# Performance work log

Measured on AMD Instinct MI355X. Metric: run time of the kernel, lower is better.

## Reference

```python
import jax, jax.numpy as jnp
import numpy as np

N_NODES = 50000
N_EDGES = 800000
IN_CH = 128
HID = 32
HEADS = 8
OUT_CH = 40
NEG_SLOPE = 0.2


def setup_inputs() -> dict:
    key = jax.random.key(0)
    ks = jax.random.split(key, 12)
    g = lambda k, shape, fan: (jax.random.normal(k, shape, jnp.float32) / np.sqrt(fan).astype(np.float32))
    return {
        "x": jax.random.normal(ks[0], (N_NODES, IN_CH), jnp.float32),
        "edge_index": jax.random.randint(ks[1], (2, N_EDGES), 0, N_NODES, jnp.int64),
        "W1l": g(ks[2], (IN_CH, HEADS * HID), IN_CH),
        "W1r": g(ks[3], (IN_CH, HEADS * HID), IN_CH),
        "att1": g(ks[4], (HEADS, HID), HID),
        "b1": jnp.zeros((HEADS * HID,), jnp.float32),
        "W2l": g(ks[5], (HEADS * HID, HID), HEADS * HID),
        "W2r": g(ks[6], (HEADS * HID, HID), HEADS * HID),
        "att2": g(ks[7], (1, HID), HID),
        "b2": jnp.zeros((HID,), jnp.float32),
        "Wc": g(ks[8], (HID + IN_CH, OUT_CH), HID + IN_CH),
        "bc": jnp.zeros((OUT_CH,), jnp.float32),
    }


def _gatv2(x, ei, Wl, Wr, att, b, heads, ch):
    # GATv2Conv (concat=True): e_ij = att . LeakyReLU(Wl x_j + Wr x_i)
    n = x.shape[0]
    src, dst = ei[0], ei[1]  # message flows src(j) -> dst(i)
    xl = (x @ Wl).reshape(n, heads, ch)  # source transform
    xr = (x @ Wr).reshape(n, heads, ch)  # target transform
    e = jax.nn.leaky_relu(xl[src] + xr[dst], NEG_SLOPE)  # [E, H, C]
    score = jnp.einsum("ehc,hc->eh", e, att)             # [E, H]
    # per-target-node segment softmax (stable)
    m = jax.ops.segment_max(score, dst, num_segments=n)
    alpha = jnp.exp(score - m[dst])
    denom = jax.ops.segment_sum(alpha, dst, num_segments=n)
    alpha = alpha / denom[dst]
    out = jax.ops.segment_sum(alpha[:, :, None] * xl[src], dst, num_segments=n)
    return out.reshape(n, heads * ch) + b


def reference(x, edge_index, W1l, W1r, att1, b1, W2l, W2r, att2, b2, Wc, bc):
    n = x.shape[0]
    ar = jnp.arange(n, dtype=edge_index.dtype)
    ei = jnp.concatenate([edge_index, jnp.stack([ar, ar])], axis=1)  # add self-loops
    h1 = jax.nn.elu(_gatv2(x, ei, W1l, W1r, att1, b1, HEADS, HID))
    h2 = jax.nn.elu(_gatv2(h1, ei, W2l, W2r, att2, b2, 1, HID))
    combined = jnp.concatenate([h2, x], axis=1)
    return combined @ Wc + bc
```

## Files before the change

### kernel.cpp

```cpp
#include <hip/hip_runtime.h>
#include <cstdint>
#include <cstddef>
#include <math.h>

#define NN 50000
#define INCH 128
#define HIDC 32
#define NHEAD 8
#define OUTC 40
#define SLOT 64

typedef unsigned short ushort_t;
using bf16x8 = __attribute__((ext_vector_type(8))) short;
using f32x4  = __attribute__((ext_vector_type(4))) float;
using f32x2  = __attribute__((ext_vector_type(2))) float;

__device__ __forceinline__ float bf2f(unsigned short h) {
    return __uint_as_float(((unsigned int)h) << 16);
}
__device__ __forceinline__ unsigned short f2bf(float f) {
    unsigned int u = __float_as_uint(f);
    u = u + 0x7FFFu + ((u >> 16) & 1u);
    return (unsigned short)(u >> 16);
}
__device__ __forceinline__ float lo16(unsigned int u) { return __uint_as_float(u << 16); }
__device__ __forceinline__ float hi16(unsigned int u) { return __uint_as_float(u & 0xffff0000u); }
__device__ __forceinline__ f32x2 up2(unsigned int u) {
    f32x2 r; r.x = lo16(u); r.y = hi16(u); return r;
}
__device__ __forceinline__ f32x2 pabs(f32x2 v) {
    return __builtin_elementwise_max(v, -v);
}

__global__ __launch_bounds__(256) void prep_all(
    const float* __restrict__ x, ushort_t* __restrict__ xb, int total8,
    const float* __restrict__ W1l, const float* __restrict__ W1r,
    const float* __restrict__ W2l, const float* __restrict__ W2r,
    const float* __restrict__ Wc,
    ushort_t* __restrict__ BT1, ushort_t* __restrict__ BT2, ushort_t* __restrict__ BTc,
    int* __restrict__ deg, int n, int CX) {
    const int blk = blockIdx.x;
    const int tid = threadIdx.x;
    if (blk < CX) {
        int i = blk * 256 + tid;
        if (i >= total8) return;
        float4 f0 = *(const float4*)(x + (size_t)i * 8);
        float4 f1 = *(const float4*)(x + (size_t)i * 8 + 4);
        ushort4 u0, u1;
        u0.x = f2bf(f0.x); u0.y = f2bf(f0.y); u0.z = f2bf(f0.z); u0.w = f2bf(f0.w);
        u1.x = f2bf(f1.x); u1.y = f2bf(f1.y); u1.z = f2bf(f1.z); u1.w = f2bf(f1.w);
        *(ushort4*)(xb + (size_t)i * 8) = u0;
        *(ushort4*)(xb + (size_t)i * 8 + 4) = u1;
    } else if (blk < CX + 616) {
        int b = blk - CX, k = tid;
        if (b < 512) {
            if (k < 128) {
                float v = (b < 256) ? W1l[(size_t)k * 256 + b] : W1r[(size_t)k * 256 + (b - 256)];
                BT1[(size_t)b * 128 + k] = f2bf(v);
            }
        } else if (b < 576) {
            int c = b - 512;
            float v = (c < 32) ? W2l[(size_t)k * 32 + c] : W2r[(size_t)k * 32 + (c - 32)];
            BT2[(size_t)c * 256 + k] = f2bf(v);
        } else {
            int c = b - 576;
            if (k < 160) BTc[(size_t)c * 160 + k] = f2bf(Wc[(size_t)k * 40 + c]);
        }
    } else {
        int i = (blk - CX - 616) * 256 + tid;
        if (i < n) deg[i] = 0;
    }
}

__global__ __launch_bounds__(256) void g1_scatter(
    const ushort_t* __restrict__ xb, const ushort_t* __restrict__ BT1,
    const float* __restrict__ att,
    ushort_t* __restrict__ xl1, ushort_t* __restrict__ xr1,
    float* __restrict__ dl, float* __restrict__ dr, int M,
    const int* __restrict__ ei, int E, int n,
    int* __restrict__ deg, int* __restrict__ csr_src, int G1) {
    const int blk = blockIdx.x;
    const int tid = threadIdx.x;
    if (blk >= G1) {
        int e = (blk - G1) * 256 + tid;
        if (e >= E + n) return;
        int src, dst;
        if (e < E) { src = ei[e]; dst = ei[E + e]; } else { src = dst = e - E; }
        int pos = atomicAdd(&deg[dst], 1);
        if (pos < SLOT) csr_src[((size_t)dst << 6) + pos] = src;
        return;
    }
    __shared__ ushort_t As[128][72];
    __shared__ ushort_t Bs[128][72];
    const int rowBase = (blk >> 2) * 128;
    const int bx = blk & 3;
    const int c0 = bx * 128;
    const int wid = tid >> 6, lane = tid & 63;
    const int wr = wid >> 1, wc = wid & 1;
    const int l15 = lane & 15, l4 = lane >> 4;
    f32x4 acc[4][4];
    #pragma unroll
    for (int i = 0; i < 4; ++i)
        #pragma unroll
        for (int j = 0; j < 4; ++j)
            #pragma unroll
            for (int q = 0; q < 4; ++q) acc[i][j][q] = 0.f;

    for (int c = 0; c < 2; ++c) {
        #pragma unroll
        for (int h = 0; h < 4; ++h) {
            int idx = h * 256 + tid;
            int r = idx >> 3, seg = idx & 7;
            int row = rowBase + r;
            uint4 v = {0, 0, 0, 0};
            if (row < M) v = *(const uint4*)(xb + (size_t)row * 128 + c * 64 + seg * 8);
            *(uint4*)&As[r][seg * 8] = v;
            *(uint4*)&Bs[r][seg * 8] = *(const uint4*)(BT1 + (size_t)(c0 + r) * 128 + c * 64 + seg * 8);
        }
        __syncthreads();
        #pragma unroll
        for (int kk = 0; kk < 2; ++kk) {
            bf16x8 a[4], b[4];
            #pragma unroll
            for (int f = 0; f < 4; ++f) {
                a[f] = *(const bf16x8*)&As[wr * 64 + f * 16 + l15][kk * 32 + l4 * 8];
                b[f] = *(const bf16x8*)&Bs[wc * 64 + f * 16 + l15][kk * 32 + l4 * 8];
            }
            #pragma unroll
            for (int i = 0; i < 4; ++i)
                #pragma unroll
                for (int j = 0; j < 4; ++j)
                    acc[i][j] = __builtin_amdgcn_mfma_f32_16x16x32_bf16(a[i], b[j], acc[i][j], 0, 0, 0);
        }
        __syncthreads();
    }
    ushort_t* __restrict__ cout = (bx < 2) ? xl1 : xr1;
    const int colBase = (bx & 1) * 128;
    #pragma unroll
    for (int i = 0; i < 4; ++i)
        #pragma unroll
        for (int r = 0; r < 4; ++r) {
            int row = rowBase + wr * 64 + i * 16 + l4 * 4 + r;
            if (row >= M) continue;
            #pragma unroll
            for (int j = 0; j < 4; ++j) {
                int col = colBase + wc * 64 + j * 16 + l15;
                cout[(size_t)row * 256 + col] = f2bf(acc[i][j][r]);
            }
        }
    float attv[4];
    #pragma unroll
    for (int j = 0; j < 4; ++j)
        attv[j] = att[(bx & 1) * 128 + wc * 64 + j * 16 + l15];
    float* __restrict__ dst = (bx < 2) ? dl : dr;
    const int headA = (bx & 1) * 4 + wc * 2;
    #pragma unroll
    for (int i = 0; i < 4; ++i)
        #pragma unroll
        for (int r = 0; r < 4; ++r) {
            float s0 = fmaf(acc[i][1][r], attv[1], acc[i][0][r] * attv[0]);
            float s1 = fmaf(acc[i][3][r], attv[3], acc[i][2][r] * attv[2]);
            s0 += __shfl_xor(s0, 1); s1 += __shfl_xor(s1, 1);
            s0 += __shfl_xor(s0, 2); s1 += __shfl_xor(s1, 2);
            s0 += __shfl_xor(s0, 4); s1 += __shfl_xor(s1, 4);
            s0 += __shfl_xor(s0, 8); s1 += __shfl_xor(s1, 8);
            if (l15 == 0) {
                int row = rowBase + wr * 64 + i * 16 + l4 * 4 + r;
                if (row < M) {
                    dst[(size_t)row * 8 + headA] = s0;
                    dst[(size_t)row * 8 + headA + 1] = s1;
                }
            }
        }
}

__global__ __launch_bounds__(256) void gat_agg1(
    const ushort_t* __restrict__ xl, const ushort_t* __restrict__ xr,
    const float* __restrict__ dl, const float* __restrict__ dr,
    const float* __restrict__ att, const float* __restrict__ b,
    const int* __restrict__ degArr, const int* __restrict__ csr_src,
    ushort_t* __restrict__ h1) {
    const int lane = threadIdx.x & 63;
    const int i = blockIdx.x * 4 + (threadIdx.x >> 6);
    const int half = lane >> 5;
    const int sl = lane & 31;
    const int head = sl >> 2;

    uint4 xv = *(const uint4*)(xr + (size_t)i * 256 + sl * 8);
    const f32x2 xr01 = up2(xv.x), xr23 = up2(xv.y), xr45 = up2(xv.z), xr67 = up2(xv.w);
    const float4 atA = *(const float4*)(att + sl * 8);
    const float4 atB = *(const float4*)(att + sl * 8 + 4);
    f32x2 at01, at23, at45, at67;
    at01.x = atA.x; at01.y = atA.y; at23.x = atA.z; at23.y = atA.w;
    at45.x = atB.x; at45.y = atB.y; at67.x = atB.z; at67.y = atB.w;
    const float cbase = 0.6f * dr[(size_t)i * 8 + head];
    int degv = degArr[i]; degv = degv < SLOT ? degv : SLOT;
    const int p0 = i << 6;
    const int p1 = p0 + degv;
    const int pfull = p0 + (degv & ~3);

    float dsum = 0.f;
    f32x2 a01 = {0.f, 0.f}, a23 = {0.f, 0.f}, a45 = {0.f, 0.f}, a67 = {0.f, 0.f};

    int pcA = p0 + half;     pcA = pcA < p1 ? pcA : p1 - 1;
    int jA = csr_src[pcA];
    uint4 uvA = *(const uint4*)(xl + (size_t)jA * 256 + sl * 8);
    float dlA = dl[(size_t)jA * 8 + head];
    int pcB = p0 + 2 + half; pcB = pcB < p1 ? pcB : p1 - 1;
    int jB = csr_src[pcB];
    uint4 uvB = *(const uint4*)(xl + (size_t)jB * 256 + sl * 8);
    float dlB = dl[(size_t)jB * 8 + head];

    for (int p = p0; p < pfull; p += 4) {
        {
            f32x2 v01 = up2(uvA.x), v23 = up2(uvA.y), v45 = up2(uvA.z), v67 = up2(uvA.w);
            float base = fmaf(0.6f, dlA, cbase);
            int nxt = p + 4 + half; int pc = nxt < p1 ? nxt : p1 - 1;
            int jn = csr_src[pc];
            uvA = *(const uint4*)(xl + (size_t)jn * 256 + sl * 8);
            dlA = dl[(size_t)jn * 8 + head];
            f32x2 q2 = at01 * pabs(v01 + xr01);
            q2 = __builtin_elementwise_fma(at23, pabs(v23 + xr23), q2);
            q2 = __builtin_elementwise_fma(at45, pabs(v45 + xr45), q2);
            q2 = __builtin_elementwise_fma(at67, pabs(v67 + xr67), q2);
            float q = q2.x + q2.y;
            q += __shfl_xor(q, 1);
            q += __shfl_xor(q, 2);
            float w = __expf(fmaf(0.4f, q, base));
            dsum += w;
            f32x2 w2; w2.x = w; w2.y = w;
            a01 = __builtin_elementwise_fma(w2, v01, a01);
            a23 = __builtin_elementwise_fma(w2, v23, a23);
            a45 = __builtin_elementwise_fma(w2, v45, a45);
            a67 = __builtin_elementwise_fma(w2, v67, a67);
        }
        {
            f32x2 v01 = up2(uvB.x), v23 = up2(uvB.y), v45 = up2(uvB.z), v67 = up2(uvB.w);
            float base = fmaf(0.6f, dlB, cbase);
            int nxt = p + 6 + half; int pc = nxt < p1 ? nxt : p1 - 1;
            int jn = csr_src[pc];
            uvB = *(const uint4*)(xl + (size_t)jn * 256 + sl * 8);
            dlB = dl[(size_t)jn * 8 + head];
            f32x2 q2 = at01 * pabs(v01 + xr01);
            q2 = __builtin_elementwise_fma(at23, pabs(v23 + xr23), q2);
            q2 = __builtin_elementwise_fma(at45, pabs(v45 + xr45), q2);
            q2 = __builtin_elementwise_fma(at67, pabs(v67 + xr67), q2);
            float q = q2.x + q2.y;
            q += __shfl_xor(q, 1);
            q += __shfl_xor(q, 2);
            float w = __expf(fmaf(0.4f, q, base));
            dsum += w;
            f32x2 w2; w2.x = w; w2.y = w;
            a01 = __builtin_elementwise_fma(w2, v01, a01);
            a23 = __builtin_elementwise_fma(w2, v23, a23);
            a45 = __builtin_elementwise_fma(w2, v45, a45);
            a67 = __builtin_elementwise_fma(w2, v67, a67);
        }
    }
    const int t = degv & 3;
    if (t) {
        {
            const bool val = half < t;
            f32x2 v01 = up2(uvA.x), v23 = up2(uvA.y), v45 = up2(uvA.z), v67 = up2(uvA.w);
            float base = fmaf(0.6f, dlA, cbase);
            f32x2 q2 = at01 * pabs(v01 + xr01);
            q2 = __builtin_elementwise_fma(at23, pabs(v23 + xr23), q2);
            q2 = __builtin_elementwise_fma(at45, pabs(v45 + xr45), q2);
            q2 = __builtin_elementwise_fma(at67, pabs(v67 + xr67), q2);
            float q = q2.x + q2.y;
            q += __shfl_xor(q, 1);
            q += __shfl_xor(q, 2);
            float w = val ? __expf(fmaf(0.4f, q, base)) : 0.f;
            dsum += w;
            f32x2 w2; w2.x = w; w2.y = w;
            a01 = __builtin_elementwise_fma(w2, v01, a01);
            a23 = __builtin_elementwise_fma(w2, v23, a23);
            a45 = __builtin_elementwise_fma(w2, v45, a45);
            a67 = __builtin_elementwise_fma(w2, v67, a67);
        }
        if (t > 2) {
            const bool val = (2 + half) < t;
            f32x2 v01 = up2(uvB.x), v23 = up2(uvB.y), v45 = up2(uvB.z), v67 = up2(uvB.w);
            float base = fmaf(0.6f, dlB, cbase);
            f32x2 q2 = at01 * pabs(v01 + xr01);
            q2 = __builtin_elementwise_fma(at23, pabs(v23 + xr23), q2);
            q2 = __builtin_elementwise_fma(at45, pabs(v45 + xr45), q2);
            q2 = __builtin_elementwise_fma(at67, pabs(v67 + xr67), q2);
            float q = q2.x + q2.y;
            q += __shfl_xor(q, 1);
            q += __shfl_xor(q, 2);
            float w = val ? __expf(fmaf(0.4f, q, base)) : 0.f;
            dsum += w;
            f32x2 w2; w2.x = w; w2.y = w;
            a01 = __builtin_elementwise_fma(w2, v01, a01);
            a23 = __builtin_elementwise_fma(w2, v23, a23);
            a45 = __builtin_elementwise_fma(w2, v45, a45);
            a67 = __builtin_elementwise_fma(w2, v67, a67);
        }
    }
    dsum += __shfl_xor(dsum, 32);
    a01.x += __shfl_xor(a01.x, 32); a01.y += __shfl_xor(a01.y, 32);
    a23.x += __shfl_xor(a23.x, 32); a23.y += __shfl_xor(a23.y, 32);
    a45.x += __shfl_xor(a45.x, 32); a45.y += __shfl_xor(a45.y, 32);
    a67.x += __shfl_xor(a67.x, 32); a67.y += __shfl_xor(a67.y, 32);

    if (half == 0) {
        const float4 bA = *(const float4*)(b + sl * 8);
        const float4 bB = *(const float4*)(b + sl * 8 + 4);
        float inv = 1.f / dsum;
        float o0 = fmaf(a01.x, inv, bA.x), o1 = fmaf(a01.y, inv, bA.y);
        float o2 = fmaf(a23.x, inv, bA.z), o3 = fmaf(a23.y, inv, bA.w);
        float o4 = fmaf(a45.x, inv, bB.x), o5 = fmaf(a45.y, inv, bB.y);
        float o6 = fmaf(a67.x, inv, bB.z), o7 = fmaf(a67.y, inv, bB.w);
        o0 = o0 > 0.f ? o0 : __expf(o0) - 1.f;
        o1 = o1 > 0.f ? o1 : __expf(o1) - 1.f;
        o2 = o2 > 0.f ? o2 : __expf(o2) - 1.f;
        o3 = o3 > 0.f ? o3 : __expf(o3) - 1.f;
        o4 = o4 > 0.f ? o4 : __expf(o4) - 1.f;
        o5 = o5 > 0.f ? o5 : __expf(o5) - 1.f;
        o6 = o6 > 0.f ? o6 : __expf(o6) - 1.f;
        o7 = o7 > 0.f ? o7 : __expf(o7) - 1.f;
        uint4 ov;
        ov.x = ((unsigned)f2bf(o1) << 16) | f2bf(o0);
        ov.y = ((unsigned)f2bf(o3) << 16) | f2bf(o2);
        ov.z = ((unsigned)f2bf(o5) << 16) | f2bf(o4);
        ov.w = ((unsigned)f2bf(o7) << 16) | f2bf(o6);
        *(uint4*)(h1 + (size_t)i * 256 + sl * 8) = ov;
    }
}

__global__ __launch_bounds__(256) void gemm2_mfma(
    const ushort_t* __restrict__ h1, const ushort_t* __restrict__ BT2,
    const float* __restrict__ att,
    ushort_t* __restrict__ xl2, ushort_t* __restrict__ xr2,
    float* __restrict__ dl2, float* __restrict__ dr2, int M) {
    __shared__ ushort_t As[128][72];
    __shared__ ushort_t Bs[64][264];
    const int tid = threadIdx.x;
    const int rowBase = blockIdx.x * 128;
    const int wid = tid >> 6, lane = tid & 63;
    const int l15 = lane & 15, l4 = lane >> 4;
    #pragma unroll
    for (int h = 0; h < 8; ++h) {
        int idx = h * 256 + tid;
        int r = idx >> 5, seg = idx & 31;
        *(uint4*)&Bs[r][seg * 8] = *(const uint4*)(BT2 + (size_t)r * 256 + seg * 8);
    }
    f32x4 acc[2][4];
    #pragma unroll
    for (int i = 0; i < 2; ++i)
        #pragma unroll
        for (int j = 0; j < 4; ++j)
            #pragma unroll
            for (int q = 0; q < 4; ++q) acc[i][j][q] = 0.f;

    for (int c = 0; c < 4; ++c) {
        #pragma unroll
        for (int h = 0; h < 4; ++h) {
            int idx = h * 256 + tid;
            int r = idx >> 3, seg = idx & 7;
            int row = rowBase + r;
            uint4 v = {0, 0, 0, 0};
            if (row < M) v = *(const uint4*)(h1 + (size_t)row * 256 + c * 64 + seg * 8);
            *(uint4*)&As[r][seg * 8] = v;
        }
        __syncthreads();
        #pragma unroll
        for (int kk = 0; kk < 2; ++kk) {
            bf16x8 a[2], b[4];
            #pragma unroll
            for (int f = 0; f < 2; ++f)
                a[f] = *(const bf16x8*)&As[wid * 32 + f * 16 + l15][kk * 32 + l4 * 8];
            #pragma unroll
            for (int f = 0; f < 4; ++f)
                b[f] = *(const bf16x8*)&Bs[f * 16 + l15][c * 64 + kk * 32 + l4 * 8];
            #pragma unroll
            for (int i = 0; i < 2; ++i)
                #pragma unroll
                for (int j = 0; j < 4; ++j)
                    acc[i][j] = __builtin_amdgcn_mfma_f32_16x16x32_bf16(a[i], b[j], acc[i][j], 0, 0, 0);
        }
        __syncthreads();
    }
    #pragma unroll
    for (int i = 0; i < 2; ++i)
        #pragma unroll
        for (int r = 0; r < 4; ++r) {
            int row = rowBase + wid * 32 + i * 16 + l4 * 4 + r;
            if (row >= M) continue;
            #pragma unroll
            for (int j = 0; j < 4; ++j) {
                int col = j * 16 + l15;
                if (col < 32) xl2[(size_t)row * 32 + col] = f2bf(acc[i][j][r]);
                else          xr2[(size_t)row * 32 + (col - 32)] = f2bf(acc[i][j][r]);
            }
        }
    float attv[4];
    #pragma unroll
    for (int j = 0; j < 4; ++j)
        attv[j] = att[(j * 16 + l15) & 31];
    #pragma unroll
    for (int i = 0; i < 2; ++i)
        #pragma unroll
        for (int r = 0; r < 4; ++r) {
            float s0 = fmaf(acc[i][1][r], attv[1], acc[i][0][r] * attv[0]);
            float s1 = fmaf(acc[i][3][r], attv[3], acc[i][2][r] * attv[2]);
            s0 += __shfl_xor(s0, 1); s1 += __shfl_xor(s1, 1);
            s0 += __shfl_xor(s0, 2); s1 += __shfl_xor(s1, 2);
            s0 += __shfl_xor(s0, 4); s1 += __shfl_xor(s1, 4);
            s0 += __shfl_xor(s0, 8); s1 += __shfl_xor(s1, 8);
            if (l15 == 0) {
                int row = rowBase + wid * 32 + i * 16 + l4 * 4 + r;
                if (row < M) {
                    dl2[row] = s0;
                    dr2[row] = s1;
                }
            }
        }
}

__global__ __launch_bounds__(256) void gat_agg2(
    const ushort_t* __restrict__ xl, const ushort_t* __restrict__ xr,
    const float* __restrict__ dl, const float* __restrict__ dr,
    const float* __restrict__ att, const float* __restrict__ b,
    const int* __restrict__ degArr, const int* __restrict__ csr_src,
    ushort_t* __restrict__ h2) {
    const int lane = threadIdx.x & 63;
    const int i = blockIdx.x * 4 + (threadIdx.x >> 6);
    const int g = lane >> 3;
    const int h8 = lane & 7;
    uint2 xv = *(const uint2*)(xr + (size_t)i * 32 + h8 * 4);
    const f32x2 xr01 = up2(xv.x), xr23 = up2(xv.y);
    const float4 at = *(const float4*)(att + h8 * 4);
    f32x2 at01, at23;
    at01.x = at.x; at01.y = at.y; at23.x = at.z; at23.y = at.w;
    const float cbase = 0.6f * dr[i];
    int degv = degArr[i]; degv = degv < SLOT ? degv : SLOT;
    const int p0 = i << 6;
    const int p1 = p0 + degv;
    const int pfull = p0 + (degv & ~15);
    float dsum = 0.f;
    f32x2 a01 = {0.f, 0.f}, a23 = {0.f, 0.f};

    int pcA = p0 + g;     pcA = pcA < p1 ? pcA : p1 - 1;
    int jA = csr_src[pcA];
    uint2 uvA = *(const uint2*)(xl + (size_t)jA * 32 + h8 * 4);
    float dlA = dl[jA];
    int pcB = p0 + g + 8; pcB = pcB < p1 ? pcB : p1 - 1;
    int jB = csr_src[pcB];
    uint2 uvB = *(const uint2*)(xl + (size_t)jB * 32 + h8 * 4);
    float dlB = dl[jB];

    for (int p = p0; p < pfull; p += 16) {
        {
            f32x2 v01 = up2(uvA.x), v23 = up2(uvA.y);
            float base = fmaf(0.6f, dlA, cbase);
            int nxt = p + g + 16; int pc = nxt < p1 ? nxt : p1 - 1;
            int jn = csr_src[pc];
            uvA = *(const uint2*)(xl + (size_t)jn * 32 + h8 * 4);
            dlA = dl[jn];
            f32x2 q2 = at01 * pabs(v01 + xr01);
            q2 = __builtin_elementwise_fma(at23, pabs(v23 + xr23), q2);
            float q = q2.x + q2.y;
            q += __shfl_xor(q, 1);
            q += __shfl_xor(q, 2);
            q += __shfl_xor(q, 4);
            float w = __expf(fmaf(0.4f, q, base));
            dsum += w;
            f32x2 w2; w2.x = w; w2.y = w;
            a01 = __builtin_elementwise_fma(w2, v01, a01);
            a23 = __builtin_elementwise_fma(w2, v23, a23);
        }
        {
            f32x2 v01 = up2(uvB.x), v23 = up2(uvB.y);
            float base = fmaf(0.6f, dlB, cbase);
            int nxt = p + g + 24; int pc = nxt < p1 ? nxt : p1 - 1;
            int jn = csr_src[pc];
            uvB = *(const uint2*)(xl + (size_t)jn * 32 + h8 * 4);
            dlB = dl[jn];
            f32x2 q2 = at01 * pabs(v01 + xr01);
            q2 = __builtin_elementwise_fma(at23, pabs(v23 + xr23), q2);
            float q = q2.x + q2.y;
            q += __shfl_xor(q, 1);
            q += __shfl_xor(q, 2);
            q += __shfl_xor(q, 4);
            float w = __expf(fmaf(0.4f, q, base));
            dsum += w;
            f32x2 w2; w2.x = w; w2.y = w;
            a01 = __builtin_elementwise_fma(w2, v01, a01);
            a23 = __builtin_elementwise_fma(w2, v23, a23);
        }
    }
    const int t = degv & 15;
    if (t) {
        {
            const bool val = g < t;
            f32x2 v01 = up2(uvA.x), v23 = up2(uvA.y);
            float base = fmaf(0.6f, dlA, cbase);
            f32x2 q2 = at01 * pabs(v01 + xr01);
            q2 = __builtin_elementwise_fma(at23, pabs(v23 + xr23), q2);
            float q = q2.x + q2.y;
            q += __shfl_xor(q, 1);
            q += __shfl_xor(q, 2);
            q += __shfl_xor(q, 4);
            float w = val ? __expf(fmaf(0.4f, q, base)) : 0.f;
            dsum += w;
            f32x2 w2; w2.x = w; w2.y = w;
            a01 = __builtin_elementwise_fma(w2, v01, a01);
            a23 = __builtin_elementwise_fma(w2, v23, a23);
        }
        if (t > 8) {
            const bool val = (g + 8) < t;
            f32x2 v01 = up2(uvB.x), v23 = up2(uvB.y);
            float base = fmaf(0.6f, dlB, cbase);
            f32x2 q2 = at01 * pabs(v01 + xr01);
            q2 = __builtin_elementwise_fma(at23, pabs(v23 + xr23), q2);
            float q = q2.x + q2.y;
            q += __shfl_xor(q, 1);
            q += __shfl_xor(q, 2);
            q += __shfl_xor(q, 4);
            float w = val ? __expf(fmaf(0.4f, q, base)) : 0.f;
            dsum += w;
            f32x2 w2; w2.x = w; w2.y = w;
            a01 = __builtin_elementwise_fma(w2, v01, a01);
            a23 = __builtin_elementwise_fma(w2, v23, a23);
        }
    }
    dsum += __shfl_xor(dsum, 8);  dsum += __shfl_xor(dsum, 16);  dsum += __shfl_xor(dsum, 32);
    a01.x += __shfl_xor(a01.x, 8); a01.x += __shfl_xor(a01.x, 16); a01.x += __shfl_xor(a01.x, 32);
    a01.y += __shfl_xor(a01.y, 8); a01.y += __shfl_xor(a01.y, 16); a01.y += __shfl_xor(a01.y, 32);
    a23.x += __shfl_xor(a23.x, 8); a23.x += __shfl_xor(a23.x, 16); a23.x += __shfl_xor(a23.x, 32);
    a23.y += __shfl_xor(a23.y, 8); a23.y += __shfl_xor(a23.y, 16); a23.y += __shfl_xor(a23.y, 32);
    if (g == 0) {
        const float4 bb = *(const float4*)(b + h8 * 4);
        float inv = 1.f / dsum;
        float o0 = fmaf(a01.x, inv, bb.x);
        float o1 = fmaf(a01.y, inv, bb.y);
        float o2 = fmaf(a23.x, inv, bb.z);
        float o3 = fmaf(a23.y, inv, bb.w);
        o0 = o0 > 0.f ? o0 : __expf(o0) - 1.f;
        o1 = o1 > 0.f ? o1 : __expf(o1) - 1.f;
        o2 = o2 > 0.f ? o2 : __expf(o2) - 1.f;
        o3 = o3 > 0.f ? o3 : __expf(o3) - 1.f;
        uint2 ov;
        ov.x = ((unsigned)f2bf(o1) << 16) | f2bf(o0);
        ov.y = ((unsigned)f2bf(o3) << 16) | f2bf(o2);
        *(uint2*)(h2 + (size_t)i * 32 + h8 * 4) = ov;
    }
}

__global__ __launch_bounds__(256) void final_mfma(
    const ushort_t* __restrict__ h2, const ushort_t* __restrict__ xb,
    const ushort_t* __restrict__ BTc, const float* __restrict__ bc,
    float* __restrict__ out, int M) {
    __shared__ ushort_t As[128][168];
    __shared__ ushort_t Bs[48][168];
    const int tid = threadIdx.x;
    const int rowBase = blockIdx.x * 128;
    const int wid = tid >> 6, lane = tid & 63;
    const int l15 = lane & 15, l4 = lane >> 4;
    #pragma unroll
    for (int h = 0; h < 4; ++h) {
        int idx = h * 256 + tid;
        if (idx < 960) {
            int r = idx / 20, seg = idx % 20;
            uint4 v = {0, 0, 0, 0};
            if (r < 40) v = *(const uint4*)(BTc + (size_t)r * 160 + seg * 8);
            *(uint4*)&Bs[r][seg * 8] = v;
        }
    }
    #pragma unroll
    for (int h = 0; h < 10; ++h) {
        int idx = h * 256 + tid;
        int r = idx / 20, seg = idx % 20;
        int row = rowBase + r;
        uint4 v = {0, 0, 0, 0};
        if (row < M)
            v = (seg < 4) ? *(const uint4*)(h2 + (size_t)row * 32 + seg * 8)
                          : *(const uint4*)(xb + (size_t)row * 128 + (seg - 4) * 8);
        *(uint4*)&As[r][seg * 8] = v;
    }
    __syncthreads();
    f32x4 acc[2][3];
    #pragma unroll
    for (int i = 0; i < 2; ++i)
        #pragma unroll
        for (int j = 0; j < 3; ++j)
            #pragma unroll
            for (int q = 0; q < 4; ++q) acc[i][j][q] = 0.f;
    #pragma unroll
    for (int kk = 0; kk < 5; ++kk) {
        bf16x8 a[2], b[3];
        #pragma unroll
        for (int f = 0; f < 2; ++f)
            a[f] = *(const bf16x8*)&As[wid * 32 + f * 16 + l15][kk * 32 + l4 * 8];
        #pragma unroll
        for (int f = 0; f < 3; ++f)
            b[f] = *(const bf16x8*)&Bs[f * 16 + l15][kk * 32 + l4 * 8];
        #pragma unroll
        for (int i = 0; i < 2; ++i)
            #pragma unroll
            for (int j = 0; j < 3; ++j)
                acc[i][j] = __builtin_amdgcn_mfma_f32_16x16x32_bf16(a[i], b[j], acc[i][j], 0, 0, 0);
    }
    #pragma unroll
    for (int i = 0; i < 2; ++i)
        #pragma unroll
        for (int r = 0; r < 4; ++r) {
            int row = rowBase + wid * 32 + i * 16 + l4 * 4 + r;
            if (row >= M) continue;
            #pragma unroll
            for (int j = 0; j < 3; ++j) {
                int col = j * 16 + l15;
                if (col < 40) out[(size_t)row * 40 + col] = acc[i][j][r] + bc[col];
            }
        }
}


extern "C" void kernel_launch(void* const* d_in, const int* in_sizes, int n_in,
                              void* d_out, int out_size, void* d_ws, size_t ws_size,
                              hipStream_t stream) {
    const float* x    = (const float*)d_in[0];
    const int*   ei   = (const int*)d_in[1];
    const float* W1l  = (const float*)d_in[2];
    const float* W1r  = (const float*)d_in[3];
    const float* att1 = (const float*)d_in[4];
    const float* b1   = (const float*)d_in[5];
    const float* W2l  = (const float*)d_in[6];
    const float* W2r  = (const float*)d_in[7];
    const float* att2 = (const float*)d_in[8];
    const float* b2   = (const float*)d_in[9];
    const float* Wc   = (const float*)d_in[10];
    const float* bc   = (const float*)d_in[11];
    float* out = (float*)d_out;

    const int n  = NN;
    const int E  = in_sizes[1] / 2;
    const int TE = E + n;
    const int CX = (n * 128 / 8 + 255) / 256;
    const int DZ = (n + 255) / 256;
    const int CD = (TE + 255) / 256;
    const int G1 = 4 * ((n + 127) / 128);

    char* ws = (char*)d_ws;
    size_t off = 0;
    auto alloc = [&](size_t bytes) { void* p = ws + off; off += (bytes + 255) & ~(size_t)255; return p; };
    ushort_t* xb   = (ushort_t*)alloc((size_t)n * 128 * 2);
    ushort_t* xl1  = (ushort_t*)alloc((size_t)n * 256 * 2);
    ushort_t* xr1  = (ushort_t*)alloc((size_t)n * 256 * 2);
    ushort_t* h1   = (ushort_t*)alloc((size_t)n * 256 * 2);
    ushort_t* xl2  = (ushort_t*)alloc((size_t)n * 32 * 2);
    ushort_t* xr2  = (ushort_t*)alloc((size_t)n * 32 * 2);
    ushort_t* h2   = (ushort_t*)alloc((size_t)n * 32 * 2);
    ushort_t* BT1  = (ushort_t*)alloc(512 * 128 * 2);
    ushort_t* BT2  = (ushort_t*)alloc(64 * 256 * 2);
    ushort_t* BTc  = (ushort_t*)alloc(40 * 160 * 2);
    float* dl1 = (float*)alloc((size_t)n * 8 * 4);
    float* dr1 = (float*)alloc((size_t)n * 8 * 4);
    float* dl2 = (float*)alloc((size_t)n * 4);
    float* dr2 = (float*)alloc((size_t)n * 4);
    int* deg     = (int*)alloc((size_t)n * 4);
    int* csr_src = (int*)alloc((size_t)n * SLOT * 4);

    prep_all<<<CX + 616 + DZ, 256, 0, stream>>>(x, xb, n * 128 / 8,
        W1l, W1r, W2l, W2r, Wc, BT1, BT2, BTc, deg, n, CX);

    g1_scatter<<<G1 + CD, 256, 0, stream>>>(xb, BT1, att1, xl1, xr1, dl1, dr1, n,
                                            ei, E, n, deg, csr_src, G1);

    gat_agg1<<<n / 4, 256, 0, stream>>>(xl1, xr1, dl1, dr1, att1, b1, deg, csr_src, h1);

    gemm2_mfma<<<(n + 127) / 128, 256, 0, stream>>>(h1, BT2, att2, xl2, xr2, dl2, dr2, n);

    gat_agg2<<<n / 4, 256, 0, stream>>>(xl2, xr2, dl2, dr2, att2, b2, deg, csr_src, h2);

    final_mfma<<<(n + 127) / 128, 256, 0, stream>>>(h2, xb, BTc, bc, out, n);
}
```

Measured before the change: 312.5 us.

## Split edge scatter from GEMM1 kernel and batch atomics per thread

Separates the fused GEMM1 plus edge-scatter kernel into two launches: a scatter kernel where each thread handles four edges with their loads and atomics issued together, and a standalone GEMM kernel on a 2D grid. Self-loops are now written in prep (deg initialised to 1 with slot 0 set), so the scatter skips n atomics. This removes divergent block roles in one kernel but adds an extra launch and serialises scatter before GEMM on the stream.

```diff
diff --git a/kernel.cpp b/kernel.cpp
--- a/kernel.cpp
+++ b/kernel.cpp
@@ -38,7 +38,7 @@
     const float* __restrict__ W2l, const float* __restrict__ W2r,
     const float* __restrict__ Wc,
     ushort_t* __restrict__ BT1, ushort_t* __restrict__ BT2, ushort_t* __restrict__ BTc,
-    int* __restrict__ deg, int n, int CX) {
+    int* __restrict__ deg, int* __restrict__ csr_src, int n, int CX) {
     const int blk = blockIdx.x;
     const int tid = threadIdx.x;
     if (blk < CX) {
@@ -68,32 +68,45 @@
         }
     } else {
         int i = (blk - CX - 616) * 256 + tid;
-        if (i < n) deg[i] = 0;
-    }
-}
-
-__global__ __launch_bounds__(256) void g1_scatter(
+        if (i < n) {
+            deg[i] = 1;
+            csr_src[(size_t)i << 6] = i;
+        }
+    }
+}
+
+__global__ __launch_bounds__(256) void scatter_edges(
+    const int* __restrict__ ei, int E,
+    int* __restrict__ deg, int* __restrict__ csr_src) {
+    const int base = blockIdx.x * 1024 + threadIdx.x;
+    int src[4], dst[4], pos[4];
+    bool ok[4];
+    #pragma unroll
+    for (int k = 0; k < 4; ++k) {
+        int e = base + k * 256;
+        ok[k] = e < E;
+        int ec = ok[k] ? e : 0;
+        src[k] = ei[ec];
+        dst[k] = ei[E + ec];
+    }
+    #pragma unroll
+    for (int k = 0; k < 4; ++k)
+        pos[k] = ok[k] ? atomicAdd(&deg[dst[k]], 1) : SLOT;
+    #pragma unroll
+    for (int k = 0; k < 4; ++k)
+        if (pos[k] < SLOT) csr_src[((size_t)dst[k] << 6) + pos[k]] = src[k];
+}
+
+__global__ __launch_bounds__(256) void gemm1_mfma(
     const ushort_t* __restrict__ xb, const ushort_t* __restrict__ BT1,
     const float* __restrict__ att,
     ushort_t* __restrict__ xl1, ushort_t* __restrict__ xr1,
-    float* __restrict__ dl, float* __restrict__ dr, int M,
-    const int* __restrict__ ei, int E, int n,
-    int* __restrict__ deg, int* __restrict__ csr_src, int G1) {
-    const int blk = blockIdx.x;
-    const int tid = threadIdx.x;
-    if (blk >= G1) {
-        int e = (blk - G1) * 256 + tid;
-        if (e >= E + n) return;
-        int src, dst;
-        if (e < E) { src = ei[e]; dst = ei[E + e]; } else { src = dst = e - E; }
-        int pos = atomicAdd(&deg[dst], 1);
-        if (pos < SLOT) csr_src[((size_t)dst << 6) + pos] = src;
-        return;
-    }
+    float* __restrict__ dl, float* __restrict__ dr, int M) {
     __shared__ ushort_t As[128][72];
     __shared__ ushort_t Bs[128][72];
-    const int rowBase = (blk >> 2) * 128;
-    const int bx = blk & 3;
+    const int tid = threadIdx.x;
+    const int rowBase = blockIdx.y * 128;
+    const int bx = blockIdx.x;
     const int c0 = bx * 128;
     const int wid = tid >> 6, lane = tid & 63;
     const int wr = wid >> 1, wc = wid & 1;
@@ -637,11 +650,9 @@
 
     const int n  = NN;
     const int E  = in_sizes[1] / 2;
-    const int TE = E + n;
     const int CX = (n * 128 / 8 + 255) / 256;
     const int DZ = (n + 255) / 256;
-    const int CD = (TE + 255) / 256;
-    const int G1 = 4 * ((n + 127) / 128);
+    const int SC = (E + 1023) / 1024;
 
     char* ws = (char*)d_ws;
     size_t off = 0;
@@ -664,10 +675,11 @@
     int* csr_src = (int*)alloc((size_t)n * SLOT * 4);
 
     prep_all<<<CX + 616 + DZ, 256, 0, stream>>>(x, xb, n * 128 / 8,
-        W1l, W1r, W2l, W2r, Wc, BT1, BT2, BTc, deg, n, CX);
-
-    g1_scatter<<<G1 + CD, 256, 0, stream>>>(xb, BT1, att1, xl1, xr1, dl1, dr1, n,
-                                            ei, E, n, deg, csr_src, G1);
+        W1l, W1r, W2l, W2r, Wc, BT1, BT2, BTc, deg, csr_src, n, CX);
+
+    scatter_edges<<<SC, 256, 0, stream>>>(ei, E, deg, csr_src);
+
+    gemm1_mfma<<<dim3(4, (n + 127) / 128), 256, 0, stream>>>(xb, BT1, att1, xl1, xr1, dl1, dr1, n);
 
     gat_agg1<<<n / 4, 256, 0, stream>>>(xl1, xr1, dl1, dr1, att1, b1, deg, csr_src, h1);
 
```

New measurement: 308.4 us. About the same (-1.3%).
